# Kernel optimization log

Measured on AMD Instinct MI355X. Metric: run time of the kernel, lower is better.

Reference implementation:

```python
import jax, jax.numpy as jnp
import numpy as np

BATCH, LENGTH, DIM = 8, 32768, 256
MAX_N_PEAKS = 400


def _make_meta():
    # deterministic per-sample peak counts in [300, 391]
    n_peaks = 300 + (np.arange(BATCH) * 13) % 101  # [300,313,...,391]
    chunk_sizes = []
    for k in n_peaks:
        base = LENGTH // (k + 1)  # guarantees trailing remainder >= base >= 1
        alt = np.where(np.arange(k) % 2 == 0, 1, -1)
        if k % 2 == 1:
            alt[-1] = 0
        sizes = base + alt  # per-peak chunk lengths, all >= 1
        trailing = LENGTH - int(sizes.sum())  # discarded padding chunk
        assert trailing >= 1
        chunk_sizes.append(np.concatenate([sizes, [trailing]]))
    chunk_size = np.concatenate(chunk_sizes).astype(np.int64)  # (total_chunks,)
    assert chunk_size.sum() == BATCH * LENGTH
    return n_peaks.astype(np.int64), chunk_size


def setup_inputs() -> dict:
    key = jax.random.key(0)
    n_peaks, chunk_size = _make_meta()
    x = jax.random.normal(key, (BATCH, LENGTH, DIM), dtype=jnp.float32)
    return {
        "x": x,
        "chunk_size": jnp.asarray(chunk_size),
        "n_peaks": jnp.asarray(n_peaks),
        "max_n_peaks": MAX_N_PEAKS,
    }


def reference(x, chunk_size, n_peaks, max_n_peaks):
    # x: (B, L, D); chunk_size: (total_chunks,) summing to B*L;
    # each sample owns n_peaks[i]+1 consecutive chunks, last one discarded.
    batch, length, dim = x.shape
    total_chunks = chunk_size.shape[0]
    flat = x.reshape(-1, dim)  # (B*L, D)
    # segment id per flattened position (static output length -> jit friendly)
    seg = jnp.repeat(jnp.arange(total_chunks), chunk_size,
                     total_repeat_length=batch * length)
    # pool_method='sum' -> segmented sum over each chunk
    sums = jax.ops.segment_sum(flat, seg, num_segments=total_chunks)  # (TC, D)
    # first chunk index of each sample
    starts = jnp.concatenate([jnp.zeros(1, dtype=n_peaks.dtype),
                              jnp.cumsum(n_peaks + 1)[:-1]])  # (B,)
    j = jnp.arange(max_n_peaks)  # (P,)
    idx = starts[:, None] + j[None, :]              # (B, P) chunk index per slot
    mask = j[None, :] < n_peaks[:, None]            # valid-peak mask
    idx = jnp.minimum(idx, total_chunks - 1)        # clamp masked-out slots
    out = jnp.where(mask[:, :, None], sums[idx], jnp.zeros((), x.dtype))
    return out  # (B, max_n_peaks, D)
```

## Files before the change

### kernel.cpp

```cpp
#include <hip/hip_runtime.h>

#define DIM 256

__global__ __launch_bounds__(256) void splitpool_wave_kernel(
    const float* __restrict__ x,
    const int* __restrict__ chunk_size,
    const int* __restrict__ n_peaks,
    float* __restrict__ out,
    int B, int L, int P, int slots)
{
    const int tid  = threadIdx.x;
    const int wave = tid >> 6;
    const int lane = tid & 63;
    const int slot = blockIdx.x * 4 + wave;
    if (slot >= slots) return;

    const int b = slot / P;
    const int j = slot - b * P;

    float4* out4 = (float4*)out + (size_t)slot * (DIM / 4) + lane;

    const int np = n_peaks[b];
    if (j >= np) {
        *out4 = make_float4(0.f, 0.f, 0.f, 0.f);
        return;
    }

    int c0 = 0;
    for (int bb = 0; bb < b; ++bb) c0 += n_peaks[bb] + 1;

    int partial = 0;
    for (int k = lane; k < j; k += 64) partial += chunk_size[c0 + k];
    #pragma unroll
    for (int m = 32; m >= 1; m >>= 1) partial += __shfl_xor(partial, m, 64);
    const int prefix = partial;
    const int nrows  = chunk_size[c0 + j];

    const float4* xp = (const float4*)x
                     + ((size_t)b * (size_t)L + (size_t)prefix) * (DIM / 4)
                     + lane;

    float4 a0 = make_float4(0.f, 0.f, 0.f, 0.f);
    float4 a1 = make_float4(0.f, 0.f, 0.f, 0.f);
    float4 a2 = make_float4(0.f, 0.f, 0.f, 0.f);
    float4 a3 = make_float4(0.f, 0.f, 0.f, 0.f);

    int r = 0;
    for (; r + 3 < nrows; r += 4) {
        float4 v0 = xp[(size_t)(r + 0) * (DIM / 4)];
        float4 v1 = xp[(size_t)(r + 1) * (DIM / 4)];
        float4 v2 = xp[(size_t)(r + 2) * (DIM / 4)];
        float4 v3 = xp[(size_t)(r + 3) * (DIM / 4)];
        a0.x += v0.x; a0.y += v0.y; a0.z += v0.z; a0.w += v0.w;
        a1.x += v1.x; a1.y += v1.y; a1.z += v1.z; a1.w += v1.w;
        a2.x += v2.x; a2.y += v2.y; a2.z += v2.z; a2.w += v2.w;
        a3.x += v3.x; a3.y += v3.y; a3.z += v3.z; a3.w += v3.w;
    }
    for (; r < nrows; ++r) {
        float4 v0 = xp[(size_t)r * (DIM / 4)];
        a0.x += v0.x; a0.y += v0.y; a0.z += v0.z; a0.w += v0.w;
    }

    a0.x += a1.x + a2.x + a3.x;
    a0.y += a1.y + a2.y + a3.y;
    a0.z += a1.z + a2.z + a3.z;
    a0.w += a1.w + a2.w + a3.w;

    *out4 = a0;
}

extern "C" void kernel_launch(void* const* d_in, const int* in_sizes, int n_in,
                              void* d_out, int out_size, void* d_ws, size_t ws_size,
                              hipStream_t stream) {
    const float* x  = (const float*)d_in[0];
    const int*   cs = (const int*)d_in[1];
    const int*   np = (const int*)d_in[2];
    float*       out = (float*)d_out;

    const int B = in_sizes[2];
    const int P = out_size / (B * DIM);
    const int L = in_sizes[0] / (B * DIM);
    const int slots = B * P;

    const int blocks = (slots + 3) / 4;
    splitpool_wave_kernel<<<dim3(blocks), 256, 0, stream>>>(
        x, cs, np, out, B, L, P, slots);
}
```

Baseline: 48.11 us.

## Split each chunk's rows across four waves per block with LDS reduction

Each output slot now gets a full 256-thread block instead of one wave. The four waves stride over the chunk's rows, interleaved by four, and their partial sums are combined through shared memory before one wave writes the result. This puts more loads in flight per chunk and spreads the work over more wavefronts. The cost is a shared-memory reduction, a barrier, and four times as many threads doing the redundant prefix-sum and mask work.

```diff
diff --git a/kernel.cpp b/kernel.cpp
--- a/kernel.cpp
+++ b/kernel.cpp
@@ -2,27 +2,25 @@
 
 #define DIM 256
 
-__global__ __launch_bounds__(256) void splitpool_wave_kernel(
+__global__ __launch_bounds__(256) void splitpool_kernel(
     const float* __restrict__ x,
     const int* __restrict__ chunk_size,
     const int* __restrict__ n_peaks,
     float* __restrict__ out,
-    int B, int L, int P, int slots)
+    int B, int L, int P)
 {
+    const int blk  = blockIdx.x;
+    const int b    = blk / P;
+    const int j    = blk - b * P;
     const int tid  = threadIdx.x;
     const int wave = tid >> 6;
     const int lane = tid & 63;
-    const int slot = blockIdx.x * 4 + wave;
-    if (slot >= slots) return;
 
-    const int b = slot / P;
-    const int j = slot - b * P;
-
-    float4* out4 = (float4*)out + (size_t)slot * (DIM / 4) + lane;
+    float4* out4 = (float4*)(out + (size_t)blk * DIM);
 
     const int np = n_peaks[b];
     if (j >= np) {
-        *out4 = make_float4(0.f, 0.f, 0.f, 0.f);
+        if (tid < DIM / 4) out4[tid] = make_float4(0.f, 0.f, 0.f, 0.f);
         return;
     }
 
@@ -45,28 +43,40 @@
     float4 a2 = make_float4(0.f, 0.f, 0.f, 0.f);
     float4 a3 = make_float4(0.f, 0.f, 0.f, 0.f);
 
-    int r = 0;
-    for (; r + 3 < nrows; r += 4) {
-        float4 v0 = xp[(size_t)(r + 0) * (DIM / 4)];
-        float4 v1 = xp[(size_t)(r + 1) * (DIM / 4)];
-        float4 v2 = xp[(size_t)(r + 2) * (DIM / 4)];
-        float4 v3 = xp[(size_t)(r + 3) * (DIM / 4)];
+    int r = wave;
+    for (; r + 12 < nrows; r += 16) {
+        float4 v0 = xp[(size_t)(r + 0)  * (DIM / 4)];
+        float4 v1 = xp[(size_t)(r + 4)  * (DIM / 4)];
+        float4 v2 = xp[(size_t)(r + 8)  * (DIM / 4)];
+        float4 v3 = xp[(size_t)(r + 12) * (DIM / 4)];
         a0.x += v0.x; a0.y += v0.y; a0.z += v0.z; a0.w += v0.w;
         a1.x += v1.x; a1.y += v1.y; a1.z += v1.z; a1.w += v1.w;
         a2.x += v2.x; a2.y += v2.y; a2.z += v2.z; a2.w += v2.w;
         a3.x += v3.x; a3.y += v3.y; a3.z += v3.z; a3.w += v3.w;
     }
-    for (; r < nrows; ++r) {
+    for (; r < nrows; r += 4) {
         float4 v0 = xp[(size_t)r * (DIM / 4)];
         a0.x += v0.x; a0.y += v0.y; a0.z += v0.z; a0.w += v0.w;
     }
-
     a0.x += a1.x + a2.x + a3.x;
     a0.y += a1.y + a2.y + a3.y;
     a0.z += a1.z + a2.z + a3.z;
     a0.w += a1.w + a2.w + a3.w;
 
-    *out4 = a0;
+    __shared__ float4 fred[256];
+    fred[tid] = a0;
+    __syncthreads();
+    if (tid < 64) {
+        float4 a  = fred[tid];
+        float4 b1 = fred[tid + 64];
+        float4 c  = fred[tid + 128];
+        float4 d  = fred[tid + 192];
+        a.x += b1.x + c.x + d.x;
+        a.y += b1.y + c.y + d.y;
+        a.z += b1.z + c.z + d.z;
+        a.w += b1.w + c.w + d.w;
+        out4[tid] = a;
+    }
 }
 
 extern "C" void kernel_launch(void* const* d_in, const int* in_sizes, int n_in,
@@ -80,9 +90,6 @@
     const int B = in_sizes[2];
     const int P = out_size / (B * DIM);
     const int L = in_sizes[0] / (B * DIM);
-    const int slots = B * P;
 
-    const int blocks = (slots + 3) / 4;
-    splitpool_wave_kernel<<<dim3(blocks), 256, 0, stream>>>(
-        x, cs, np, out, B, L, P, slots);
+    splitpool_kernel<<<dim3(B * P), 256, 0, stream>>>(x, cs, np, out, B, L, P);
 }
```

Measured after the change: 45.38 us. 1.06x faster.
